# Optimization experiments

Hardware: AMD Instinct MI355X
Metric: run time of the kernel (lower is better)

The kernel has to match this reference:

```python
import jax, jax.numpy as jnp
import numpy as np

B, T, D, K = 4, 2048, 1024, 4

def setup_inputs() -> dict:
    key = jax.random.key(0)
    ks = jax.random.split(key, 4)
    u = jax.random.normal(ks[0], (B, T, D), dtype=jnp.float32)
    s0 = jnp.zeros((B, K, D), dtype=jnp.float32)
    W_in = jax.random.normal(ks[1], (K * D, D), dtype=jnp.float32) * (1.0 / np.sqrt(D))
    b_in = jnp.zeros((K * D,), dtype=jnp.float32)
    W_out = jax.random.normal(ks[2], (D, K * D), dtype=jnp.float32) * (1.0 / np.sqrt(K * D))
    b_out = jnp.zeros((D,), dtype=jnp.float32)
    decay_logit = jax.random.normal(ks[3], (K,), dtype=jnp.float32)
    return {"u": u, "s0": s0, "W_in": W_in, "b_in": b_in,
            "W_out": W_out, "b_out": b_out, "decay_logit": decay_logit}

def reference(u, s0, W_in, b_in, W_out, b_out, decay_logit):
    # u: (B,T,D); s0: (B,K,D)
    Bb, Tt, Dd = u.shape
    Kk = decay_logit.shape[0]
    # input projection -> (B,T,K,D) -> (T,B,K,D) for scan over time
    inp = (jnp.einsum('btd,ed->bte', u, W_in) + b_in).reshape(Bb, Tt, Kk, Dd)
    xs = jnp.transpose(inp, (1, 0, 2, 3))  # (T,B,K,D)
    decay = jax.nn.sigmoid(decay_logit).reshape(1, Kk, 1)  # (1,K,1)

    def step(s, x):
        s_next = decay * s + x
        return s_next, s_next

    s_last, s_seq = jax.lax.scan(step, s0, xs)  # s_seq: (T,B,K,D)
    g_in = jnp.transpose(s_seq, (1, 0, 2, 3)).reshape(Bb, Tt, Kk * Dd)
    g = jnp.einsum('bte,de->btd', g_in, W_out) + b_out
    return g, s_last
```

## Files before the change

### kernel.cpp

```cpp
#include <hip/hip_runtime.h>


#define Bb 4
#define Tt 2048
#define Dd 1024
#define Kk 4
#define BT (Bb*Tt)
#define Ee (Kk*Dd)
#define NCH 32
#define LCH 64

typedef __bf16 bf16x8 __attribute__((ext_vector_type(8)));
typedef float  f32x4  __attribute__((ext_vector_type(4)));

__device__ __forceinline__ float bf2f(ushort u){
  union { unsigned int i; float f; } x; x.i = ((unsigned int)u) << 16; return x.f;
}
__device__ __forceinline__ ushort f2bf(float f){
  union { unsigned int i; float f; } x; x.f = f;
  unsigned int i = x.i;
  return (ushort)((i + 0x7FFFu + ((i >> 16) & 1u)) >> 16);
}
__device__ __forceinline__ float sigm(float x){ return 1.0f / (1.0f + expf(-x)); }

__global__ __launch_bounds__(256) void k_f2bf4(const float4* __restrict__ in,
                                               ushort4* __restrict__ out, int n4){
  int i = blockIdx.x * 256 + threadIdx.x;
  if (i < n4){
    float4 v = in[i];
    ushort4 o; o.x = f2bf(v.x); o.y = f2bf(v.y); o.z = f2bf(v.z); o.w = f2bf(v.w);
    out[i] = o;
  }
}

__global__ __launch_bounds__(256) void k_transpose(const float* __restrict__ in,
                                                   ushort* __restrict__ out){
  __shared__ float tile[32][33];
  int tx = threadIdx.x, ty = threadIdx.y;
  int c0 = blockIdx.x * 32, r0 = blockIdx.y * 32;
  #pragma unroll
  for (int j = 0; j < 4; ++j)
    tile[ty + j*8][tx] = in[(size_t)(r0 + ty + j*8) * Dd + c0 + tx];
  __syncthreads();
  #pragma unroll
  for (int j = 0; j < 4; ++j)
    out[(size_t)(c0 + ty + j*8) * Ee + r0 + tx] = f2bf(tile[tx][ty + j*8]);
}

__global__ __launch_bounds__(256) void gemm_nt(const ushort* __restrict__ A,
                                               const ushort* __restrict__ B,
                                               ushort* __restrict__ C,
                                               int Kred, int lda, int ldb, int ldc,
                                               long aBatch, long bBatch, long cBatch){
  __shared__ ushort As[128 * 32];
  __shared__ ushort Bs[128 * 32];
  A += (long)blockIdx.z * aBatch;
  B += (long)blockIdx.z * bBatch;
  C += (long)blockIdx.z * cBatch;
  const int tid  = threadIdx.x;
  const int lane = tid & 63;
  const int w    = tid >> 6;
  const int wr   = w >> 1, wc = w & 1;
  const int rowBase = blockIdx.x * 128;
  const int colBase = blockIdx.y * 128;

  f32x4 acc[4][4] = {};
  const int krow = (lane >> 4) * 8;
  const int rsel = lane & 15;

  for (int kk = 0; kk < Kred; kk += 32){
    __syncthreads();
    #pragma unroll
    for (int i = 0; i < 2; ++i){
      int c  = i * 256 + tid;
      int r  = c >> 2;
      int c8 = (c & 3) * 8;
      const ushort* ga = A + (size_t)(rowBase + r) * lda + kk + c8;
      const ushort* gb = B + (size_t)(colBase + r) * ldb + kk + c8;
      __builtin_amdgcn_global_load_lds((const __attribute__((address_space(1))) void*)ga,
                                       (__attribute__((address_space(3))) void*)&As[c * 8],
                                       16, 0, 0);
      __builtin_amdgcn_global_load_lds((const __attribute__((address_space(1))) void*)gb,
                                       (__attribute__((address_space(3))) void*)&Bs[c * 8],
                                       16, 0, 0);
    }
    asm volatile("s_waitcnt vmcnt(0)" ::: "memory");
    __syncthreads();

    bf16x8 Af[4], Bf[4];
    #pragma unroll
    for (int mi = 0; mi < 4; ++mi)
      Af[mi] = *(const bf16x8*)&As[(wr*64 + mi*16 + rsel) * 32 + krow];
    #pragma unroll
    for (int ni = 0; ni < 4; ++ni)
      Bf[ni] = *(const bf16x8*)&Bs[(wc*64 + ni*16 + rsel) * 32 + krow];
    #pragma unroll
    for (int mi = 0; mi < 4; ++mi)
      #pragma unroll
      for (int ni = 0; ni < 4; ++ni)
        acc[mi][ni] = __builtin_amdgcn_mfma_f32_16x16x32_bf16(Af[mi], Bf[ni], acc[mi][ni], 0, 0, 0);
  }

  #pragma unroll
  for (int mi = 0; mi < 4; ++mi){
    #pragma unroll
    for (int ni = 0; ni < 4; ++ni){
      int r0 = rowBase + wr*64 + mi*16 + (lane >> 4) * 4;
      int c0 = colBase + wc*64 + ni*16 + (lane & 15);
      #pragma unroll
      for (int q = 0; q < 4; ++q)
        C[(size_t)(r0 + q) * ldc + c0] = f2bf(acc[mi][ni][q]);
    }
  }
}

#define STAGE_HALF(GB, LOFF)                                                   \
  { _Pragma("unroll")                                                          \
    for (int i_ = 0; i_ < 2; ++i_){                                            \
      int c_ = tid + i_*512;                                                   \
      int row_ = c_ >> 2;                                                      \
      int ss_ = (c_ & 3) ^ ((row_ >> 2) & 3);                                  \
      const ushort* g_ = (GB) + (size_t)row_ * 1024 + ss_ * 8;                 \
      __builtin_amdgcn_global_load_lds(                                        \
        (const __attribute__((address_space(1))) void*)g_,                     \
        (__attribute__((address_space(3))) void*)&lds[(LOFF) + c_*8],          \
        16, 0, 0);                                                             \
    } }

#define LDA_FRAGS(KH)                                                          \
  { _Pragma("unroll")                                                          \
    for (int mi_ = 0; mi_ < 8; ++mi_){                                         \
      int r_ = wm*128 + mi_*16 + rsel;                                         \
      int uo_ = r_*32 + kq*8;                                                  \
      uo_ ^= ((uo_ >> 7) & 3) << 3;                                            \
      af[mi_] = *(const bf16x8*)&lds[cbase + (KH)*8192 + uo_];                 \
    } }

#define LDB_FRAGS(KH, NH)                                                      \
  { _Pragma("unroll")                                                          \
    for (int ni_ = 0; ni_ < 2; ++ni_){                                         \
      int r_ = wn*64 + (NH)*32 + ni_*16 + rsel;                                \
      int uo_ = r_*32 + kq*8;                                                  \
      uo_ ^= ((uo_ >> 7) & 3) << 3;                                            \
      bfr[ni_] = *(const bf16x8*)&lds[cbase + 16384 + (KH)*8192 + uo_];        \
    } }

#define MFMA_PH(NH)                                                            \
  { __builtin_amdgcn_s_setprio(1);                                             \
    _Pragma("unroll")                                                          \
    for (int mi_ = 0; mi_ < 8; ++mi_)                                          \
      { _Pragma("unroll")                                                      \
        for (int ni_ = 0; ni_ < 2; ++ni_)                                      \
          acc[mi_][(NH)*2+ni_] = __builtin_amdgcn_mfma_f32_16x16x32_bf16(      \
              af[mi_], bfr[ni_], acc[mi_][(NH)*2+ni_], 0, 0, 0); }             \
    __builtin_amdgcn_s_setprio(0); }

#define BAR() __builtin_amdgcn_s_barrier()

__global__ __launch_bounds__(512, 2) void gemm_big(const ushort* __restrict__ A,
                                                   const ushort* __restrict__ B,
                                                   ushort* __restrict__ C){
  __shared__ ushort lds[65536];
  const int tid  = threadIdx.x;
  const int lane = tid & 63;
  const int w    = tid >> 6;
  const int wm   = w >> 2;
  const int wn   = w & 3;
  const int rsel = lane & 15;
  const int kq   = lane >> 4;

  int bid = blockIdx.x;
  int swz = (bid & 7) * 64 + (bid >> 3);
  const int rowBase = (swz & 31) * 256;
  const int colBase = (swz >> 5) * 256;

  const ushort* Ag = A + (size_t)rowBase * 1024;
  const ushort* Bg = B + (size_t)colBase * 1024;

  f32x4 acc[8][4] = {};
  bf16x8 af[8], bfr[2];

  STAGE_HALF(Ag +  0, 0);
  STAGE_HALF(Bg +  0, 16384);
  STAGE_HALF(Ag + 32, 8192);
  STAGE_HALF(Bg + 32, 24576);
  STAGE_HALF(Ag + 64, 32768 + 0);
  STAGE_HALF(Bg + 64, 32768 + 16384);
  STAGE_HALF(Ag + 96, 32768 + 8192);
  asm volatile("s_waitcnt vmcnt(6)" ::: "memory");
  BAR();

  for (int t = 0; t < 16; ++t){
    const int cbase = (t & 1) * 32768;
    const int obase = cbase ^ 32768;
    LDA_FRAGS(0); LDB_FRAGS(0, 0);
    if (t + 1 < 16) STAGE_HALF(Bg + (t+1)*64 + 32, obase + 24576);
    BAR();
    MFMA_PH(0);
    BAR();
    LDB_FRAGS(0, 1);
    if (t + 2 < 16) STAGE_HALF(Ag + (t+2)*64, cbase + 0);
    BAR();
    MFMA_PH(1);
    BAR();
    LDA_FRAGS(1); LDB_FRAGS(1, 0);
    if (t + 2 < 16) STAGE_HALF(Bg + (t+2)*64, cbase + 16384);
    BAR();
    MFMA_PH(0);
    BAR();
    LDB_FRAGS(1, 1);
    if (t + 2 < 16) STAGE_HALF(Ag + (t+2)*64 + 32, cbase + 8192);
    BAR();
    MFMA_PH(1);
    if (t + 2 < 16) { asm volatile("s_waitcnt vmcnt(6)" ::: "memory"); }
    else            { asm volatile("s_waitcnt vmcnt(0)" ::: "memory"); }
    BAR();
  }

  #pragma unroll
  for (int mi = 0; mi < 8; ++mi){
    int r0 = rowBase + wm*128 + mi*16 + (lane >> 4) * 4;
    #pragma unroll
    for (int j = 0; j < 4; ++j){
      int c0 = colBase + wn*64 + j*16 + rsel;
      #pragma unroll
      for (int q = 0; q < 4; ++q)
        C[(size_t)(r0 + q) * Ee + c0] = f2bf(acc[mi][j][q]);
    }
  }
}

__global__ __launch_bounds__(256) void k_z0(const float* __restrict__ Wout,
                                            const float* __restrict__ s0,
                                            float* __restrict__ z0){
  int gid  = blockIdx.x * 4 + (threadIdx.x >> 6);
  int lane = threadIdx.x & 63;
  int d = gid & 1023, k = (gid >> 10) & 3, b = gid >> 12;
  const float* wrow = Wout + (size_t)d * Ee + k * Dd;
  const float* sv   = s0 + ((size_t)(b*Kk + k) << 10);
  float s = 0.f;
  #pragma unroll
  for (int j = 0; j < 16; ++j) s += wrow[lane + j*64] * sv[lane + j*64];
  for (int off = 32; off; off >>= 1) s += __shfl_down(s, off);
  if (lane == 0) z0[gid] = s;
}

__global__ __launch_bounds__(256) void k_cterm(const float* __restrict__ Wout,
                                               const float* __restrict__ b_in,
                                               float* __restrict__ cterm){
  int gid  = blockIdx.x * 4 + (threadIdx.x >> 6);
  int lane = threadIdx.x & 63;
  int d = gid & 1023, k = gid >> 10;
  const float* wrow = Wout + (size_t)d * Ee + k * Dd;
  const float* bv   = b_in + k * Dd;
  float s = 0.f;
  #pragma unroll
  for (int j = 0; j < 16; ++j) s += wrow[lane + j*64] * bv[lane + j*64];
  for (int off = 32; off; off >>= 1) s += __shfl_down(s, off);
  if (lane == 0) cterm[gid] = s;
}

__global__ __launch_bounds__(256) void k_scanA(const ushort* __restrict__ Y,
                                               const float* __restrict__ dlog,
                                               float* __restrict__ carry){
  int x = blockIdx.x;
  int d = blockIdx.y * 256 + threadIdx.x;
  int c = x & 31, k = (x >> 5) & 3, b = x >> 7;
  float p = sigm(dlog[k]);
  float acc = 0.f;
  size_t base = ((size_t)(b*Tt + c*LCH)) * Ee + k * Dd + d;
  for (int i = 0; i < LCH; ++i){ acc = p * acc + bf2f(Y[base]); base += Ee; }
  carry[(size_t)x * Dd + d] = acc;
}

__global__ __launch_bounds__(256) void k_scanInc(const float* __restrict__ carry,
                                                 const float* __restrict__ z0,
                                                 const float* __restrict__ dlog,
                                                 float* __restrict__ incoming){
  int idx = blockIdx.x * 256 + threadIdx.x;
  int k = (idx >> 10) & 3;
  int bk = idx >> 10, d = idx & 1023;
  float p  = sigm(dlog[k]);
  float dL = powf(p, (float)LCH);
  float inc = z0[idx];
  for (int c = 0; c < NCH; ++c){
    size_t o = ((size_t)(bk * NCH + c)) * Dd + d;
    incoming[o] = inc;
    inc = dL * inc + carry[o];
  }
}

__global__ __launch_bounds__(256) void k_scanB(const ushort* __restrict__ Y,
                                               const float* __restrict__ incoming,
                                               const float* __restrict__ dlog,
                                               const float* __restrict__ b_out,
                                               const float* __restrict__ cterm,
                                               float* __restrict__ g){
  int x = blockIdx.x;
  int d = blockIdx.y * 256 + threadIdx.x;
  int c = x & 31, b = x >> 5;
  float p[4], z[4], ct[4], pw[4];
  #pragma unroll
  for (int k = 0; k < 4; ++k){
    p[k]  = sigm(dlog[k]);
    z[k]  = incoming[((size_t)(((b*Kk + k))*NCH + c)) * Dd + d];
    float omp = fmaxf(1.0f - p[k], 1e-30f);
    ct[k] = cterm[k * Dd + d] / omp;
    pw[k] = powf(p[k], (float)(c * LCH + 1));
  }
  float bo = b_out[d];
  size_t ybase = ((size_t)(b*Tt + c*LCH)) * Ee + d;
  size_t gbase = ((size_t)(b*Tt + c*LCH)) * Dd + d;
  for (int i = 0; i < LCH; ++i){
    float acc = bo;
    #pragma unroll
    for (int k = 0; k < 4; ++k){
      z[k] = p[k] * z[k] + bf2f(Y[ybase + (size_t)k * Dd]);
      acc += z[k] + ct[k] * (1.0f - pw[k]);
      pw[k] *= p[k];
    }
    g[gbase] = acc;
    ybase += Ee; gbase += Dd;
  }
}

__global__ __launch_bounds__(256) void k_prep(const float* __restrict__ u,
                                              const float* __restrict__ dlog,
                                              float* __restrict__ vpart,
                                              ushort* __restrict__ U_bf){
  int x = blockIdx.x;
  int d = blockIdx.y * 256 + threadIdx.x;
  int c = x & 31, b = x >> 5;
  float p[4], a[4] = {0.f, 0.f, 0.f, 0.f};
  #pragma unroll
  for (int k = 0; k < 4; ++k) p[k] = sigm(dlog[k]);
  size_t ub = ((size_t)(b*Tt + c*LCH)) * Dd + d;
  for (int i = 0; i < LCH; ++i){
    float uv = u[ub];
    U_bf[ub] = f2bf(uv);
    #pragma unroll
    for (int k = 0; k < 4; ++k) a[k] = p[k] * a[k] + uv;
    ub += Dd;
  }
  #pragma unroll
  for (int k = 0; k < 4; ++k)
    vpart[(((size_t)x) * Kk + k) * Dd + d] = a[k];
}

__global__ __launch_bounds__(256) void k_vcomb(const float* __restrict__ vpart,
                                               const float* __restrict__ dlog,
                                               float* __restrict__ vfull){
  int idx = blockIdx.x * 256 + threadIdx.x;
  int k = (idx >> 10) & 3, b = idx >> 12, d = idx & 1023;
  float p  = sigm(dlog[k]);
  float dL = powf(p, (float)LCH);
  float v = 0.f;
  for (int c = 0; c < NCH; ++c)
    v = dL * v + vpart[(((size_t)(b*NCH + c)) * Kk + k) * Dd + d];
  vfull[idx] = v;
}

__global__ __launch_bounds__(256) void k_slast(const float* __restrict__ W_in,
                                               const float* __restrict__ vfull,
                                               const float* __restrict__ s0,
                                               const float* __restrict__ b_in,
                                               const float* __restrict__ dlog,
                                               float* __restrict__ out){
  int gid  = blockIdx.x * 4 + (threadIdx.x >> 6);
  int lane = threadIdx.x & 63;
  int d = gid & 1023, k = (gid >> 10) & 3, b = gid >> 12;
  const float* wrow = W_in + (size_t)(k*Dd + d) * Dd;
  const float* vv   = vfull + ((size_t)(b*Kk + k) << 10);
  float s = 0.f;
  #pragma unroll
  for (int j = 0; j < 16; ++j) s += wrow[lane + j*64] * vv[lane + j*64];
  for (int off = 32; off; off >>= 1) s += __shfl_down(s, off);
  if (lane == 0){
    float p  = sigm(dlog[k]);
    float pT = powf(p, (float)Tt);
    float omp = 1.0f - p;
    float geo = (omp < 1e-12f) ? (float)Tt : (1.0f - pT) / omp;
    out[gid] = pT * s0[gid] + s + b_in[k*Dd + d] * geo;
  }
}

extern "C" void kernel_launch(void* const* d_in, const int* in_sizes, int n_in,
                              void* d_out, int out_size, void* d_ws, size_t ws_size,
                              hipStream_t stream){
  const float* u     = (const float*)d_in[0];
  const float* s0    = (const float*)d_in[1];
  const float* W_in  = (const float*)d_in[2];
  const float* b_in  = (const float*)d_in[3];
  const float* W_out = (const float*)d_in[4];
  const float* b_out = (const float*)d_in[5];
  const float* dlog  = (const float*)d_in[6];

  float* g_out     = (float*)d_out;
  float* slast_out = g_out + (size_t)BT * Dd;

  char* ws = (char*)d_ws;
  if (ws_size < 115490816ull) return;
  ushort* U_bf    = (ushort*)(ws);
  ushort* WinT    = (ushort*)(ws + 16777216);
  ushort* Wout_bf = (ushort*)(ws + 25165824);
  ushort* Mcat    = (ushort*)(ws + 33554432);
  ushort* Y       = (ushort*)(ws + 41943040);
  float*  carry   = (float*)(ws + 109051904);
  float*  incoming= (float*)(ws + 111149056);
  float*  z0buf   = (float*)(ws + 113246208);
  float*  cterm   = (float*)(ws + 113311744);
  float*  vpart   = (float*)(ws + 113328128);
  float*  vfull   = (float*)(ws + 115425280);

  k_prep<<<dim3(128, 4), 256, 0, stream>>>(u, dlog, vpart, U_bf);
  k_f2bf4<<<4096, 256, 0, stream>>>((const float4*)W_out, (ushort4*)Wout_bf, Dd*Ee/4);
  k_transpose<<<dim3(32, 128), dim3(32, 8), 0, stream>>>(W_in, WinT);

  gemm_nt<<<dim3(8, 8, 4), 256, 0, stream>>>(Wout_bf, WinT, Mcat,
                                             1024, Ee, Ee, Dd,
                                             1024L, 1024L, 1048576L);
  gemm_big<<<512, 512, 0, stream>>>(U_bf, Mcat, Y);

  k_z0<<<4096, 256, 0, stream>>>(W_out, s0, z0buf);
  k_cterm<<<1024, 256, 0, stream>>>(W_out, b_in, cterm);

  k_scanA<<<dim3(512, 4), 256, 0, stream>>>(Y, dlog, carry);
  k_scanInc<<<64, 256, 0, stream>>>(carry, z0buf, dlog, incoming);
  k_scanB<<<dim3(128, 4), 256, 0, stream>>>(Y, incoming, dlog, b_out, cterm, g_out);

  k_vcomb<<<64, 256, 0, stream>>>(vpart, dlog, vfull);
  k_slast<<<4096, 256, 0, stream>>>(W_in, vfull, s0, b_in, dlog, slast_out);
}
```

Before: 182.6 us.

## Fuse chunk-carry scan into GEMM epilogue via LDS-staged output tile

The GEMM epilogue now writes the bf16 output tile into swizzled LDS. Each block computes the per-chunk decayed scan carries directly from that tile, then writes the tile to global memory with 16-byte vector stores. This removes the separate k_scanA kernel and its full re-read of Y. The block-to-tile mapping is also changed so each XCD covers a contiguous 8x8 group of tiles. The cost is a serial 64-step loop in the epilogue plus an extra barrier.

```diff
diff --git a/kernel.cpp b/kernel.cpp
--- a/kernel.cpp
+++ b/kernel.cpp
@@ -159,7 +159,9 @@
 
 __global__ __launch_bounds__(512, 2) void gemm_big(const ushort* __restrict__ A,
                                                    const ushort* __restrict__ B,
-                                                   ushort* __restrict__ C){
+                                                   ushort* __restrict__ C,
+                                                   const float* __restrict__ dlog,
+                                                   float* __restrict__ carry){
   __shared__ ushort lds[65536];
   const int tid  = threadIdx.x;
   const int lane = tid & 63;
@@ -170,9 +172,9 @@
   const int kq   = lane >> 4;
 
   int bid = blockIdx.x;
-  int swz = (bid & 7) * 64 + (bid >> 3);
-  const int rowBase = (swz & 31) * 256;
-  const int colBase = (swz >> 5) * 256;
+  int xcd = bid & 7, rr = bid >> 3;
+  const int rowBase = (((xcd >> 1) << 3) + (rr & 7)) * 256;
+  const int colBase = (((xcd & 1) << 3) + (rr >> 3)) * 256;
 
   const ushort* Ag = A + (size_t)rowBase * 1024;
   const ushort* Bg = B + (size_t)colBase * 1024;
@@ -219,14 +221,49 @@
 
   #pragma unroll
   for (int mi = 0; mi < 8; ++mi){
-    int r0 = rowBase + wm*128 + mi*16 + (lane >> 4) * 4;
     #pragma unroll
     for (int j = 0; j < 4; ++j){
-      int c0 = colBase + wn*64 + j*16 + rsel;
       #pragma unroll
-      for (int q = 0; q < 4; ++q)
-        C[(size_t)(r0 + q) * Ee + c0] = f2bf(acc[mi][j][q]);
+      for (int q = 0; q < 4; ++q){
+        int row = wm*128 + mi*16 + (lane >> 4)*4 + q;
+        int col = wn*64 + j*16 + rsel;
+        int byte = row*512 + col*2;
+        byte ^= ((row >> 2) & 3) << 5;
+        *(ushort*)((char*)lds + byte) = f2bf(acc[mi][j][q]);
+      }
     }
+  }
+  __syncthreads();
+
+  {
+    const int k_blk = colBase >> 10;
+    const int b_blk = rowBase >> 11;
+    const int ch0   = (rowBase & 2047) >> 6;
+    const int d0    = colBase & 1023;
+    const float p   = sigm(dlog[k_blk]);
+    #pragma unroll
+    for (int s = 0; s < 2; ++s){
+      int task = tid + s*512;
+      int col = task & 255, ch = task >> 8;
+      float a = 0.f;
+      for (int i = 0; i < 64; ++i){
+        int row = ch*64 + i;
+        int byte = row*512 + col*2;
+        byte ^= ((row >> 2) & 3) << 5;
+        a = p * a + bf2f(*(const ushort*)((char*)lds + byte));
+      }
+      carry[(size_t)((b_blk*Kk + k_blk)*NCH + ch0 + ch) * Dd + d0 + col] = a;
+    }
+  }
+
+  #pragma unroll
+  for (int j = 0; j < 16; ++j){
+    int idx = tid + j*512;
+    int r = idx >> 5, c8 = idx & 31;
+    int byte = r*512 + c8*16;
+    byte ^= ((r >> 2) & 3) << 5;
+    f32x4 v = *(const f32x4*)((char*)lds + byte);
+    *(f32x4*)&C[(size_t)(rowBase + r) * Ee + colBase + c8*8] = v;
   }
 }
 
@@ -258,19 +295,6 @@
   for (int j = 0; j < 16; ++j) s += wrow[lane + j*64] * bv[lane + j*64];
   for (int off = 32; off; off >>= 1) s += __shfl_down(s, off);
   if (lane == 0) cterm[gid] = s;
-}
-
-__global__ __launch_bounds__(256) void k_scanA(const ushort* __restrict__ Y,
-                                               const float* __restrict__ dlog,
-                                               float* __restrict__ carry){
-  int x = blockIdx.x;
-  int d = blockIdx.y * 256 + threadIdx.x;
-  int c = x & 31, k = (x >> 5) & 3, b = x >> 7;
-  float p = sigm(dlog[k]);
-  float acc = 0.f;
-  size_t base = ((size_t)(b*Tt + c*LCH)) * Ee + k * Dd + d;
-  for (int i = 0; i < LCH; ++i){ acc = p * acc + bf2f(Y[base]); base += Ee; }
-  carry[(size_t)x * Dd + d] = acc;
 }
 
 __global__ __launch_bounds__(256) void k_scanInc(const float* __restrict__ carry,
@@ -419,12 +443,11 @@
   gemm_nt<<<dim3(8, 8, 4), 256, 0, stream>>>(Wout_bf, WinT, Mcat,
                                              1024, Ee, Ee, Dd,
                                              1024L, 1024L, 1048576L);
-  gemm_big<<<512, 512, 0, stream>>>(U_bf, Mcat, Y);
+  gemm_big<<<512, 512, 0, stream>>>(U_bf, Mcat, Y, dlog, carry);
 
   k_z0<<<4096, 256, 0, stream>>>(W_out, s0, z0buf);
   k_cterm<<<1024, 256, 0, stream>>>(W_out, b_in, cterm);
 
-  k_scanA<<<dim3(512, 4), 256, 0, stream>>>(Y, dlog, carry);
   k_scanInc<<<64, 256, 0, stream>>>(carry, z0buf, dlog, incoming);
   k_scanB<<<dim3(128, 4), 256, 0, stream>>>(Y, incoming, dlog, b_out, cterm, g_out);
 
```

After: 170.9 us. -6.4%, faster.
